# Kernel tuning notes

Measured on AMD Instinct MI355X. Metric: run time of the kernel, lower is better.

## Reference

```python
import jax, jax.numpy as jnp
import numpy as np

B, T, C, H = 4, 2048, 768, 12
HD = C // H
EPS = 1e-5

def _ln(x, s, b):
    m = jnp.mean(x, axis=-1, keepdims=True)
    v = jnp.mean(jnp.square(x - m), axis=-1, keepdims=True)
    return (x - m) * jax.lax.rsqrt(v + EPS) * s + b

def setup_inputs() -> dict:
    key = jax.random.key(0)
    ks = jax.random.split(key, 8)
    x = jax.random.normal(ks[0], (B, T, C), dtype=jnp.float32)
    mask = jnp.tril(jnp.ones((T, T), dtype=bool))[None, None, :, :]  # causal [1,1,T,T]
    s = lambda fan_in: 1.0 / np.sqrt(fan_in)
    return {
        "x": x,
        "mask": mask,
        "ln1_s": jnp.ones((C,), jnp.float32),
        "ln1_b": jnp.zeros((C,), jnp.float32),
        "w_attn": jax.random.normal(ks[1], (C, 3 * C), jnp.float32) * s(C),
        "b_attn": jnp.zeros((3 * C,), jnp.float32),
        "w_o": jax.random.normal(ks[2], (C, C), jnp.float32) * s(C),
        "b_o": jnp.zeros((C,), jnp.float32),
        "ln2_s": jnp.ones((C,), jnp.float32),
        "ln2_b": jnp.zeros((C,), jnp.float32),
        "w_fc": jax.random.normal(ks[3], (C, 4 * C), jnp.float32) * s(C),
        "b_fc": jnp.zeros((4 * C,), jnp.float32),
        "w_proj": jax.random.normal(ks[4], (4 * C, C), jnp.float32) * s(4 * C),
        "b_proj": jnp.zeros((C,), jnp.float32),
    }

def reference(x, mask, ln1_s, ln1_b, w_attn, b_attn, w_o, b_o,
              ln2_s, ln2_b, w_fc, b_fc, w_proj, b_proj):
    # --- attention branch (pre-LN) ---
    h = _ln(x, ln1_s, ln1_b)
    qkv = (h @ w_attn + b_attn).reshape(B, T, 3 * H, HD)
    q, k, v = jnp.array_split(qkv, 3, axis=2)  # each [B,T,H,HD]
    scale = 1.0 / jnp.sqrt(jnp.float32(HD))
    attn = jnp.einsum('bqhd,bkhd->bhqk', q, k) * scale
    attn = jnp.where(mask, attn, jnp.finfo(jnp.float32).min)
    attn = jax.nn.softmax(attn, axis=-1)
    ctx = jnp.einsum('bhqk,bkhd->bqhd', attn, v).reshape(B, T, C)
    x = x + ctx @ w_o + b_o
    # --- MLP branch (pre-LN) ---
    h = _ln(x, ln2_s, ln2_b)
    h = jax.nn.gelu(h @ w_fc + b_fc, approximate=True)
    x = x + h @ w_proj + b_proj
    return x
```

## Files before the change

### kernel.cpp

```cpp
#include <hip/hip_runtime.h>


typedef unsigned short u16;
typedef unsigned int u32;
typedef __attribute__((ext_vector_type(8))) short short8;
typedef __attribute__((ext_vector_type(4))) float f32x4;
typedef __attribute__((ext_vector_type(16))) float f32x16;

__device__ __forceinline__ u16 f2bf(float f) {
    union { float f; unsigned u; } v; v.f = f;
    unsigned u = v.u;
    unsigned r = (u + 0x7FFFu + ((u >> 16) & 1u)) >> 16;
    return (u16)r;
}
__device__ __forceinline__ float bf2f(u16 h) {
    union { u32 u; float f; } v; v.u = ((u32)h) << 16;
    return v.f;
}

__device__ __forceinline__ u32 cvtpk_bf16(float lo, float hi) {
    u32 r;
    asm("v_cvt_pk_bf16_f32 %0, %1, %2" : "=v"(r) : "v"(lo), "v"(hi));
    return r;
}

__device__ __forceinline__ void gld16(const u16* g, u16* l) {
    __builtin_amdgcn_global_load_lds(
        (const __attribute__((address_space(1))) void*)g,
        (__attribute__((address_space(3))) void*)l, 16, 0, 0);
}

__device__ __forceinline__ float gelu_fast(float v) {
    float t = v * v;
    float z2n = v * (-2.3022078f - 0.10294376f * t);
    float e = __builtin_amdgcn_exp2f(z2n);
    return v * __builtin_amdgcn_rcpf(1.0f + e);
}

__device__ __forceinline__ void ln_core(float v0, float v1, float v2,
                                        const float* __restrict__ s,
                                        const float* __restrict__ b,
                                        u16* __restrict__ orow,
                                        float* red, int tid) {
    float sum = v0 + v1 + v2;
    float sq = v0 * v0 + v1 * v1 + v2 * v2;
#pragma unroll
    for (int off = 32; off; off >>= 1) {
        sum += __shfl_down(sum, off);
        sq += __shfl_down(sq, off);
    }
    int wid = tid >> 6, lane = tid & 63;
    if (lane == 0) { red[wid] = sum; red[4 + wid] = sq; }
    __syncthreads();
    if (tid == 0) {
        float s4 = red[0] + red[1] + red[2] + red[3];
        float q4 = red[4] + red[5] + red[6] + red[7];
        red[0] = s4 * (1.0f / 768.0f);
        red[1] = q4 * (1.0f / 768.0f);
    }
    __syncthreads();
    float mean = red[0];
    float var = red[1] - mean * mean;
    float rstd = rsqrtf(var + 1e-5f);
    orow[tid]       = f2bf((v0 - mean) * rstd * s[tid]       + b[tid]);
    orow[tid + 256] = f2bf((v1 - mean) * rstd * s[tid + 256] + b[tid + 256]);
    orow[tid + 512] = f2bf((v2 - mean) * rstd * s[tid + 512] + b[tid + 512]);
}

__global__ void pre_kernel(const float* __restrict__ w_attn, u16* __restrict__ wT_attn,
                           const float* __restrict__ w_o,    u16* __restrict__ wT_o,
                           const float* __restrict__ w_fc,   u16* __restrict__ wT_fc,
                           const float* __restrict__ w_proj, u16* __restrict__ wT_proj,
                           const float* __restrict__ x, const float* __restrict__ ln1_s,
                           const float* __restrict__ ln1_b, u16* __restrict__ h) {
    __shared__ float t[32][33];
    __shared__ float red[8];
    int tile = blockIdx.x;
    int tid = threadIdx.x;
    if (tile >= 6912) {
        int row = tile - 6912;
        const float* xr = x + (size_t)row * 768;
        ln_core(xr[tid], xr[tid + 256], xr[tid + 512], ln1_s, ln1_b,
                h + (size_t)row * 768, red, tid);
        return;
    }
    const float* w; u16* wt; int N; int idx;
    if (tile < 1728)      { w = w_attn; wt = wT_attn; N = 2304; idx = tile; }
    else if (tile < 2304) { w = w_o;    wt = wT_o;    N = 768;  idx = tile - 1728; }
    else if (tile < 4608) { w = w_fc;   wt = wT_fc;   N = 3072; idx = tile - 2304; }
    else                  { w = w_proj; wt = wT_proj; N = 768;  idx = tile - 4608; }
    int K = (tile >= 4608) ? 3072 : 768;
    int nx = N / 32;
    int n0 = (idx % nx) * 32, k0 = (idx / nx) * 32;
    int tx = tid & 31, ty = tid >> 5;
#pragma unroll
    for (int i = 0; i < 4; i++)
        t[ty + 8 * i][tx] = w[(size_t)(k0 + ty + 8 * i) * N + n0 + tx];
    __syncthreads();
#pragma unroll
    for (int i = 0; i < 4; i++)
        wt[(size_t)(n0 + ty + 8 * i) * K + k0 + tx] = f2bf(t[tx][ty + 8 * i]);
}

__global__ void ln_bf16_kernel(const u16* __restrict__ x, const float* __restrict__ s,
                               const float* __restrict__ b, u16* __restrict__ out) {
    __shared__ float red[8];
    int row = blockIdx.x;
    int tid = threadIdx.x;
    const u16* xr = x + (size_t)row * 768;
    ln_core(bf2f(xr[tid]), bf2f(xr[tid + 256]), bf2f(xr[tid + 512]),
            s, b, out + (size_t)row * 768, red, tid);
}

template <int GELU, int RES, int RESBF, int OUTMODE, int BM>
__global__ __launch_bounds__(256) void gemm_kernel(
    const u16* __restrict__ A, const u16* __restrict__ Wt,
    const float* __restrict__ bias, const void* __restrict__ res,
    void* __restrict__ out, int M, int N, int K,
    u16* __restrict__ qbuf, u16* __restrict__ kbuf, u16* __restrict__ vbuf) {
    constexpr int FM = BM / 32;
    constexpr int SA = BM / 32;
    constexpr int WR = BM / 2;
    __shared__ __align__(16) u16 lA[2][BM * 64];
    __shared__ __align__(16) u16 lB[2][128 * 64];
    int m0 = blockIdx.x * BM, n0 = blockIdx.y * 128;
    int tid = threadIdx.x;
    int wid = tid >> 6, lane = tid & 63;
    int wr = wid >> 1, wc = wid & 1;
    int l15 = lane & 15, lhi = lane >> 4;

    const u16* aptr[SA];
    const u16* bptr[4];
#pragma unroll
    for (int s = 0; s < SA; s++) {
        int u = s * 256 + tid;
        int row = u >> 3;
        int c8 = (u & 7) ^ (row & 7);
        aptr[s] = A + (size_t)(m0 + row) * K + c8 * 8;
    }
#pragma unroll
    for (int s = 0; s < 4; s++) {
        int u = s * 256 + tid;
        int row = u >> 3;
        int c8 = (u & 7) ^ (row & 7);
        bptr[s] = Wt + (size_t)(n0 + row) * K + c8 * 8;
    }

    f32x4 acc[FM][4];
#pragma unroll
    for (int i = 0; i < FM; i++)
#pragma unroll
        for (int j = 0; j < 4; j++) acc[i][j] = (f32x4)0.0f;

#pragma unroll
    for (int s = 0; s < SA; s++) gld16(aptr[s], &lA[0][(s * 256 + tid) * 8]);
#pragma unroll
    for (int s = 0; s < 4; s++) gld16(bptr[s], &lB[0][(s * 256 + tid) * 8]);
    __syncthreads();

    int KT = K >> 6;
    int cur = 0;
    for (int t = 0; t < KT; t++) {
        if (t + 1 < KT) {
            int ko = (t + 1) << 6;
#pragma unroll
            for (int s = 0; s < SA; s++) gld16(aptr[s] + ko, &lA[cur ^ 1][(s * 256 + tid) * 8]);
#pragma unroll
            for (int s = 0; s < 4; s++) gld16(bptr[s] + ko, &lB[cur ^ 1][(s * 256 + tid) * 8]);
        }
        short8 af[2][FM], bfr[2][4];
#pragma unroll
        for (int ks = 0; ks < 2; ks++) {
#pragma unroll
            for (int f = 0; f < FM; f++) {
                int ra = wr * WR + f * 16 + l15;
                af[ks][f] = *(const short8*)&lA[cur][ra * 64 + (((ks * 4 + lhi) ^ (ra & 7)) << 3)];
            }
#pragma unroll
            for (int f = 0; f < 4; f++) {
                int rb = wc * 64 + f * 16 + l15;
                bfr[ks][f] = *(const short8*)&lB[cur][rb * 64 + (((ks * 4 + lhi) ^ (rb & 7)) << 3)];
            }
        }
        __builtin_amdgcn_s_setprio(1);
#pragma unroll
        for (int ks = 0; ks < 2; ks++)
#pragma unroll
            for (int fm = 0; fm < FM; fm++)
#pragma unroll
                for (int fn = 0; fn < 4; fn++)
                    acc[fm][fn] = __builtin_amdgcn_mfma_f32_16x16x32_bf16(
                        af[ks][fm], bfr[ks][fn], acc[fm][fn], 0, 0, 0);
        __builtin_amdgcn_s_setprio(0);
        __syncthreads();
        cur ^= 1;
    }

    if (OUTMODE == 2) {
        int region = n0 / 768;
#pragma unroll
        for (int fm = 0; fm < FM; fm++)
#pragma unroll
            for (int fn = 0; fn < 4; fn++) {
                int col = n0 + wc * 64 + fn * 16 + l15;
                float bv = bias[col];
                int c = col - region * 768;
                int h = c >> 6, d = c & 63;
                if (region == 2) {
                    int row0 = m0 + wr * WR + fm * 16 + lhi * 4;
                    int bb = row0 >> 11, t0 = row0 & 2047;
                    size_t bh = (size_t)bb * 12 + h;
                    union { u16 a[4]; uint2 v; } pk;
#pragma unroll
                    for (int r = 0; r < 4; r++) pk.a[r] = f2bf(acc[fm][fn][r] + bv);
                    *(uint2*)(&vbuf[(bh * 64 + d) * 2048 + t0]) = pk.v;
                } else {
#pragma unroll
                    for (int r = 0; r < 4; r++) {
                        int row = m0 + wr * WR + fm * 16 + lhi * 4 + r;
                        int bb = row >> 11, t = row & 2047;
                        u16 val = f2bf(acc[fm][fn][r] + bv);
                        size_t bh = (size_t)bb * 12 + h;
                        if (region == 0) qbuf[(bh * 2048 + t) * 64 + d] = val;
                        else             kbuf[(bh * 2048 + t) * 64 + d] = val;
                    }
                }
            }
    } else {
#pragma unroll
        for (int fm = 0; fm < FM; fm++)
#pragma unroll
            for (int fn = 0; fn < 4; fn++) {
                int col = n0 + wc * 64 + fn * 16 + l15;
                float bv = bias[col];
#pragma unroll
                for (int r = 0; r < 4; r++) {
                    int row = m0 + wr * WR + fm * 16 + lhi * 4 + r;
                    float v = acc[fm][fn][r] + bv;
                    if (RES) {
                        if (RESBF) v += bf2f(((const u16*)res)[(size_t)row * N + col]);
                        else       v += ((const float*)res)[(size_t)row * N + col];
                    }
                    if (GELU) v = gelu_fast(v);
                    if (OUTMODE == 1)
                        ((u16*)out)[(size_t)row * N + col] = f2bf(v);
                    else
                        ((float*)out)[(size_t)row * N + col] = v;
                }
            }
    }
}

__global__ __launch_bounds__(128) void attn_kernel(const u16* __restrict__ qbuf,
                                                   const u16* __restrict__ kbuf,
                                                   const u16* __restrict__ vbuf,
                                                   u16* __restrict__ ctx) {
    int bid = blockIdx.x;
    int qt = 31 - (bid / 48);
    int bh = bid % 48;
    int b = bh / 12, h = bh % 12;
    int q0 = qt * 64;
    int tid = threadIdx.x, wid = tid >> 6, lane = tid & 63;
    int l31 = lane & 31, hi = lane >> 5;

    __shared__ __align__(16) u16 lK[2][64 * 64];
    __shared__ __align__(16) u16 lV[2][64 * 64];

    const size_t bhT = (size_t)bh * 2048;

    const u16* kp[4];
    const u16* vp[4];
#pragma unroll
    for (int s = 0; s < 4; s++) {
        int u = s * 128 + tid;
        int row = u >> 3;
        int c8 = (u & 7) ^ (row & 7);
        kp[s] = kbuf + (bhT + row) * 64 + c8 * 8;
        vp[s] = vbuf + ((size_t)bh * 64 + row) * 2048 + c8 * 8;
    }

    int qrow = q0 + wid * 32 + l31;
    short8 bq[4];
#pragma unroll
    for (int ks = 0; ks < 4; ks++)
        bq[ks] = *(const short8*)(qbuf + (bhT + qrow) * 64 + ks * 16 + hi * 8);

    short8 ones;
#pragma unroll
    for (int j = 0; j < 8; j++) ones[j] = (short)0x3F80;

    f32x16 oacc[2], sacc;
#pragma unroll
    for (int dt = 0; dt < 2; dt++) oacc[dt] = (f32x16)0.0f;
    sacc = (f32x16)0.0f;
    float mb = -1e30f;
    const float C2 = 0.125f * 1.44269504089f;
    const float THR = 11.55f;
    int myq = q0 + wid * 32 + l31;

    int nt = qt + 1;
#pragma unroll
    for (int s = 0; s < 4; s++) gld16(kp[s], &lK[0][(s * 128 + tid) * 8]);
#pragma unroll
    for (int s = 0; s < 4; s++) gld16(vp[s], &lV[0][(s * 128 + tid) * 8]);
    __syncthreads();

    int cur = 0;
    for (int t = 0; t < nt; t++) {
        int k0 = t * 64;
        if (t + 1 < nt) {
            int kn = (t + 1) * 64;
#pragma unroll
            for (int s = 0; s < 4; s++) gld16(kp[s] + (size_t)kn * 64, &lK[cur ^ 1][(s * 128 + tid) * 8]);
#pragma unroll
            for (int s = 0; s < 4; s++) gld16(vp[s] + kn, &lV[cur ^ 1][(s * 128 + tid) * 8]);
        }
        {
            f32x16 sa[2];
#pragma unroll
            for (int kt = 0; kt < 2; kt++) sa[kt] = (f32x16)0.0f;
            __builtin_amdgcn_s_setprio(1);
#pragma unroll
            for (int kt = 0; kt < 2; kt++) {
                int rk = kt * 32 + l31;
#pragma unroll
                for (int ks = 0; ks < 4; ks++) {
                    short8 ak = *(const short8*)&lK[cur][rk * 64 + (((ks * 2 + hi) ^ (rk & 7)) << 3)];
                    sa[kt] = __builtin_amdgcn_mfma_f32_32x32x16_bf16(ak, bq[ks], sa[kt], 0, 0, 0);
                }
            }
            __builtin_amdgcn_s_setprio(0);
            if (k0 + 63 > q0 + wid * 32) {
#pragma unroll
                for (int kt = 0; kt < 2; kt++)
#pragma unroll
                    for (int r = 0; r < 16; r++) {
                        int key = k0 + kt * 32 + (r & 3) + 8 * (r >> 2) + 4 * hi;
                        if (key > myq) sa[kt][r] = -1e30f;
                    }
            }
            float tmax = -1e30f;
#pragma unroll
            for (int kt = 0; kt < 2; kt++)
#pragma unroll
                for (int r = 0; r < 16; r += 2)
                    tmax = fmaxf(tmax, fmaxf(sa[kt][r], sa[kt][r + 1]));
            tmax = fmaxf(tmax, __shfl_xor(tmax, 32));
            float tmb = tmax * C2;
            if (__any(tmb > mb + THR)) {
                float mbn = fmaxf(mb, tmb);
                float corr = __builtin_amdgcn_exp2f(mb - mbn);
#pragma unroll
                for (int r = 0; r < 16; r++) {
                    int qm = (r & 3) + 8 * (r >> 2) + 4 * hi;
                    float c = __shfl(corr, qm);
                    oacc[0][r] *= c;
                    oacc[1][r] *= c;
                    sacc[r] *= c;
                }
                mb = mbn;
            }
#pragma unroll
            for (int kt = 0; kt < 2; kt++)
#pragma unroll
                for (int r = 0; r < 16; r++)
                    sa[kt][r] = __builtin_amdgcn_exp2f(fmaf(sa[kt][r], C2, -mb));
            short8 pa[4];
#pragma unroll
            for (int kt = 0; kt < 2; kt++)
#pragma unroll
                for (int ks2 = 0; ks2 < 2; ks2++) {
                    int base = ks2 * 8;
                    u32 A0 = cvtpk_bf16(sa[kt][base + 0], sa[kt][base + 1]);
                    u32 B0 = cvtpk_bf16(sa[kt][base + 4], sa[kt][base + 5]);
                    u32 A1 = cvtpk_bf16(sa[kt][base + 2], sa[kt][base + 3]);
                    u32 B1 = cvtpk_bf16(sa[kt][base + 6], sa[kt][base + 7]);
                    u32 A0s = (u32)__shfl_xor((int)A0, 32);
                    u32 B0s = (u32)__shfl_xor((int)B0, 32);
                    u32 A1s = (u32)__shfl_xor((int)A1, 32);
                    u32 B1s = (u32)__shfl_xor((int)B1, 32);
                    union { u32 u[4]; short8 s; } w;
                    w.u[0] = hi ? B0s : A0;
                    w.u[1] = hi ? B1s : A1;
                    w.u[2] = hi ? B0 : A0s;
                    w.u[3] = hi ? B1 : A1s;
                    pa[kt * 2 + ks2] = w.s;
                }
            __builtin_amdgcn_s_setprio(1);
#pragma unroll
            for (int kt = 0; kt < 2; kt++)
#pragma unroll
                for (int ks2 = 0; ks2 < 2; ks2++) {
                    short8 ap = pa[kt * 2 + ks2];
#pragma unroll
                    for (int dt = 0; dt < 2; dt++) {
                        int rd = dt * 32 + l31;
                        short8 bv = *(const short8*)&lV[cur][rd * 64 + (((kt * 4 + ks2 * 2 + hi) ^ (rd & 7)) << 3)];
                        oacc[dt] = __builtin_amdgcn_mfma_f32_32x32x16_bf16(ap, bv, oacc[dt], 0, 0, 0);
                    }
                    sacc = __builtin_amdgcn_mfma_f32_32x32x16_bf16(ap, ones, sacc, 0, 0, 0);
                }
            __builtin_amdgcn_s_setprio(0);
        }
        __syncthreads();
        cur ^= 1;
    }
    const size_t rowb = (size_t)b * 2048;
#pragma unroll
    for (int r = 0; r < 16; r++) {
        float ir = __builtin_amdgcn_rcpf(sacc[r]);
        int qm = (r & 3) + 8 * (r >> 2) + 4 * hi;
        int row = q0 + wid * 32 + qm;
        u16* op = ctx + (rowb + row) * 768 + h * 64 + l31;
        op[0]  = f2bf(oacc[0][r] * ir);
        op[32] = f2bf(oacc[1][r] * ir);
    }
}

extern "C" void kernel_launch(void* const* d_in, const int* in_sizes, int n_in,
                              void* d_out, int out_size, void* d_ws, size_t ws_size,
                              hipStream_t stream) {
    const float* x      = (const float*)d_in[0];
    const float* ln1_s  = (const float*)d_in[2];
    const float* ln1_b  = (const float*)d_in[3];
    const float* w_attn = (const float*)d_in[4];
    const float* b_attn = (const float*)d_in[5];
    const float* w_o    = (const float*)d_in[6];
    const float* b_o    = (const float*)d_in[7];
    const float* ln2_s  = (const float*)d_in[8];
    const float* ln2_b  = (const float*)d_in[9];
    const float* w_fc   = (const float*)d_in[10];
    const float* b_fc   = (const float*)d_in[11];
    const float* w_proj = (const float*)d_in[12];
    const float* b_proj = (const float*)d_in[13];

    char* ws = (char*)d_ws;
    u16* wT_attn = (u16*)(ws + 0);
    u16* wT_o    = (u16*)(ws + 3538944);
    u16* wT_fc   = (u16*)(ws + 4718592);
    u16* wT_proj = (u16*)(ws + 9437184);
    u16* bufA    = (u16*)(ws + 14155776);
    u16* qbuf    = (u16*)(ws + 26738688);
    u16* kbuf    = (u16*)(ws + 39321600);
    u16* vbuf    = (u16*)(ws + 51904512);
    u16* act     = (u16*)(ws + 26738688);
    u16* x1b     = (u16*)(ws + 77070336);

    pre_kernel<<<15104, 256, 0, stream>>>(w_attn, wT_attn, w_o, wT_o, w_fc, wT_fc,
                                          w_proj, wT_proj, x, ln1_s, ln1_b, bufA);
    gemm_kernel<0, 0, 0, 2, 128><<<dim3(64, 18), 256, 0, stream>>>(bufA, wT_attn, b_attn, nullptr, nullptr,
                                                                   8192, 2304, 768, qbuf, kbuf, vbuf);
    attn_kernel<<<1536, 128, 0, stream>>>(qbuf, kbuf, vbuf, bufA);
    gemm_kernel<0, 1, 0, 1, 64><<<dim3(128, 6), 256, 0, stream>>>(bufA, wT_o, b_o, x, x1b,
                                                                  8192, 768, 768, nullptr, nullptr, nullptr);
    ln_bf16_kernel<<<8192, 256, 0, stream>>>(x1b, ln2_s, ln2_b, bufA);
    gemm_kernel<1, 0, 0, 1, 128><<<dim3(64, 24), 256, 0, stream>>>(bufA, wT_fc, b_fc, nullptr, act,
                                                                   8192, 3072, 768, nullptr, nullptr, nullptr);
    gemm_kernel<0, 1, 1, 0, 64><<<dim3(128, 6), 256, 0, stream>>>(act, wT_proj, b_proj, x1b, (float*)d_out,
                                                                  8192, 768, 3072, nullptr, nullptr, nullptr);
}
```

Baseline: 252.6 us.

## Load attention K tiles directly into registers instead of shared memory

The attention kernel no longer stages K through double-buffered LDS. Each lane loads its MFMA A-operand fragments for the next K tile straight from global memory into a register double-buffer (ak0/ak1), alternating by tile parity. V is still staged through LDS. This removes the LDS write/read traffic for K and frees LDS, but it raises register pressure (16 short8 held live) and duplicates global K loads across the two waves, which may lower occupancy or expose load latency.

```diff
diff --git a/kernel.cpp b/kernel.cpp
--- a/kernel.cpp
+++ b/kernel.cpp
@@ -263,21 +263,19 @@
     int tid = threadIdx.x, wid = tid >> 6, lane = tid & 63;
     int l31 = lane & 31, hi = lane >> 5;
 
-    __shared__ __align__(16) u16 lK[2][64 * 64];
     __shared__ __align__(16) u16 lV[2][64 * 64];
 
     const size_t bhT = (size_t)bh * 2048;
 
-    const u16* kp[4];
     const u16* vp[4];
 #pragma unroll
     for (int s = 0; s < 4; s++) {
         int u = s * 128 + tid;
         int row = u >> 3;
         int c8 = (u & 7) ^ (row & 7);
-        kp[s] = kbuf + (bhT + row) * 64 + c8 * 8;
         vp[s] = vbuf + ((size_t)bh * 64 + row) * 2048 + c8 * 8;
     }
+    const u16* kb = kbuf + bhT * 64 + (size_t)l31 * 64 + hi * 8;
 
     int qrow = q0 + wid * 32 + l31;
     short8 bq[4];
@@ -299,112 +297,120 @@
     int myq = q0 + wid * 32 + l31;
 
     int nt = qt + 1;
-#pragma unroll
-    for (int s = 0; s < 4; s++) gld16(kp[s], &lK[0][(s * 128 + tid) * 8]);
-#pragma unroll
-    for (int s = 0; s < 4; s++) gld16(vp[s], &lV[0][(s * 128 + tid) * 8]);
-    __syncthreads();
+    short8 ak0[8], ak1[8];
+
+    auto loadK = [&](short8* ak, int k0) {
+#pragma unroll
+        for (int kt = 0; kt < 2; kt++)
+#pragma unroll
+            for (int ks = 0; ks < 4; ks++)
+                ak[kt * 4 + ks] = *(const short8*)(kb + (size_t)(k0 + kt * 32) * 64 + ks * 16);
+    };
 
     int cur = 0;
-    for (int t = 0; t < nt; t++) {
+    auto tile_body = [&](short8* akC, short8* akN, int t) {
         int k0 = t * 64;
         if (t + 1 < nt) {
             int kn = (t + 1) * 64;
-#pragma unroll
-            for (int s = 0; s < 4; s++) gld16(kp[s] + (size_t)kn * 64, &lK[cur ^ 1][(s * 128 + tid) * 8]);
+            loadK(akN, kn);
 #pragma unroll
             for (int s = 0; s < 4; s++) gld16(vp[s] + kn, &lV[cur ^ 1][(s * 128 + tid) * 8]);
         }
-        {
-            f32x16 sa[2];
-#pragma unroll
-            for (int kt = 0; kt < 2; kt++) sa[kt] = (f32x16)0.0f;
-            __builtin_amdgcn_s_setprio(1);
-#pragma unroll
-            for (int kt = 0; kt < 2; kt++) {
-                int rk = kt * 32 + l31;
-#pragma unroll
-                for (int ks = 0; ks < 4; ks++) {
-                    short8 ak = *(const short8*)&lK[cur][rk * 64 + (((ks * 2 + hi) ^ (rk & 7)) << 3)];
-                    sa[kt] = __builtin_amdgcn_mfma_f32_32x32x16_bf16(ak, bq[ks], sa[kt], 0, 0, 0);
+        f32x16 sa[2];
+#pragma unroll
+        for (int kt = 0; kt < 2; kt++) sa[kt] = (f32x16)0.0f;
+        __builtin_amdgcn_s_setprio(1);
+#pragma unroll
+        for (int kt = 0; kt < 2; kt++)
+#pragma unroll
+            for (int ks = 0; ks < 4; ks++)
+                sa[kt] = __builtin_amdgcn_mfma_f32_32x32x16_bf16(akC[kt * 4 + ks], bq[ks], sa[kt], 0, 0, 0);
+        __builtin_amdgcn_s_setprio(0);
+        if (k0 + 63 > q0 + wid * 32) {
+#pragma unroll
+            for (int kt = 0; kt < 2; kt++)
+#pragma unroll
+                for (int r = 0; r < 16; r++) {
+                    int key = k0 + kt * 32 + (r & 3) + 8 * (r >> 2) + 4 * hi;
+                    if (key > myq) sa[kt][r] = -1e30f;
                 }
-            }
-            __builtin_amdgcn_s_setprio(0);
-            if (k0 + 63 > q0 + wid * 32) {
-#pragma unroll
-                for (int kt = 0; kt < 2; kt++)
-#pragma unroll
-                    for (int r = 0; r < 16; r++) {
-                        int key = k0 + kt * 32 + (r & 3) + 8 * (r >> 2) + 4 * hi;
-                        if (key > myq) sa[kt][r] = -1e30f;
-                    }
-            }
-            float tmax = -1e30f;
-#pragma unroll
-            for (int kt = 0; kt < 2; kt++)
-#pragma unroll
-                for (int r = 0; r < 16; r += 2)
-                    tmax = fmaxf(tmax, fmaxf(sa[kt][r], sa[kt][r + 1]));
-            tmax = fmaxf(tmax, __shfl_xor(tmax, 32));
-            float tmb = tmax * C2;
-            if (__any(tmb > mb + THR)) {
-                float mbn = fmaxf(mb, tmb);
-                float corr = __builtin_amdgcn_exp2f(mb - mbn);
-#pragma unroll
-                for (int r = 0; r < 16; r++) {
-                    int qm = (r & 3) + 8 * (r >> 2) + 4 * hi;
-                    float c = __shfl(corr, qm);
-                    oacc[0][r] *= c;
-                    oacc[1][r] *= c;
-                    sacc[r] *= c;
+        }
+        float tmax = -1e30f;
+#pragma unroll
+        for (int kt = 0; kt < 2; kt++)
+#pragma unroll
+            for (int r = 0; r < 16; r += 2)
+                tmax = fmaxf(tmax, fmaxf(sa[kt][r], sa[kt][r + 1]));
+        tmax = fmaxf(tmax, __shfl_xor(tmax, 32));
+        float tmb = tmax * C2;
+        if (__any(tmb > mb + THR)) {
+            float mbn = fmaxf(mb, tmb);
+            float corr = __builtin_amdgcn_exp2f(mb - mbn);
+#pragma unroll
+            for (int r = 0; r < 16; r++) {
+                int qm = (r & 3) + 8 * (r >> 2) + 4 * hi;
+                float c = __shfl(corr, qm);
+                oacc[0][r] *= c;
+                oacc[1][r] *= c;
+                sacc[r] *= c;
+            }
+            mb = mbn;
+        }
+#pragma unroll
+        for (int kt = 0; kt < 2; kt++)
+#pragma unroll
+            for (int r = 0; r < 16; r++)
+                sa[kt][r] = __builtin_amdgcn_exp2f(fmaf(sa[kt][r], C2, -mb));
+        short8 pa[4];
+#pragma unroll
+        for (int kt = 0; kt < 2; kt++)
+#pragma unroll
+            for (int ks2 = 0; ks2 < 2; ks2++) {
+                int base = ks2 * 8;
+                u32 A0 = cvtpk_bf16(sa[kt][base + 0], sa[kt][base + 1]);
+                u32 B0 = cvtpk_bf16(sa[kt][base + 4], sa[kt][base + 5]);
+                u32 A1 = cvtpk_bf16(sa[kt][base + 2], sa[kt][base + 3]);
+                u32 B1 = cvtpk_bf16(sa[kt][base + 6], sa[kt][base + 7]);
+                u32 A0s = (u32)__shfl_xor((int)A0, 32);
+                u32 B0s = (u32)__shfl_xor((int)B0, 32);
+                u32 A1s = (u32)__shfl_xor((int)A1, 32);
+                u32 B1s = (u32)__shfl_xor((int)B1, 32);
+                union { u32 u[4]; short8 s; } w;
+                w.u[0] = hi ? B0s : A0;
+                w.u[1] = hi ? B1s : A1;
+                w.u[2] = hi ? B0 : A0s;
+                w.u[3] = hi ? B1 : A1s;
+                pa[kt * 2 + ks2] = w.s;
+            }
+        __builtin_amdgcn_s_setprio(1);
+#pragma unroll
+        for (int kt = 0; kt < 2; kt++)
+#pragma unroll
+            for (int ks2 = 0; ks2 < 2; ks2++) {
+                short8 ap = pa[kt * 2 + ks2];
+#pragma unroll
+                for (int dt = 0; dt < 2; dt++) {
+                    int rd = dt * 32 + l31;
+                    short8 bv = *(const short8*)&lV[cur][rd * 64 + (((kt * 4 + ks2 * 2 + hi) ^ (rd & 7)) << 3)];
+                    oacc[dt] = __builtin_amdgcn_mfma_f32_32x32x16_bf16(ap, bv, oacc[dt], 0, 0, 0);
                 }
-                mb = mbn;
-            }
-#pragma unroll
-            for (int kt = 0; kt < 2; kt++)
-#pragma unroll
-                for (int r = 0; r < 16; r++)
-                    sa[kt][r] = __builtin_amdgcn_exp2f(fmaf(sa[kt][r], C2, -mb));
-            short8 pa[4];
-#pragma unroll
-            for (int kt = 0; kt < 2; kt++)
-#pragma unroll
-                for (int ks2 = 0; ks2 < 2; ks2++) {
-                    int base = ks2 * 8;
-                    u32 A0 = cvtpk_bf16(sa[kt][base + 0], sa[kt][base + 1]);
-                    u32 B0 = cvtpk_bf16(sa[kt][base + 4], sa[kt][base + 5]);
-                    u32 A1 = cvtpk_bf16(sa[kt][base + 2], sa[kt][base + 3]);
-                    u32 B1 = cvtpk_bf16(sa[kt][base + 6], sa[kt][base + 7]);
-                    u32 A0s = (u32)__shfl_xor((int)A0, 32);
-                    u32 B0s = (u32)__shfl_xor((int)B0, 32);
-                    u32 A1s = (u32)__shfl_xor((int)A1, 32);
-                    u32 B1s = (u32)__shfl_xor((int)B1, 32);
-                    union { u32 u[4]; short8 s; } w;
-                    w.u[0] = hi ? B0s : A0;
-                    w.u[1] = hi ? B1s : A1;
-                    w.u[2] = hi ? B0 : A0s;
-                    w.u[3] = hi ? B1 : A1s;
-                    pa[kt * 2 + ks2] = w.s;
-                }
-            __builtin_amdgcn_s_setprio(1);
-#pragma unroll
-            for (int kt = 0; kt < 2; kt++)
-#pragma unroll
-                for (int ks2 = 0; ks2 < 2; ks2++) {
-                    short8 ap = pa[kt * 2 + ks2];
-#pragma unroll
-                    for (int dt = 0; dt < 2; dt++) {
-                        int rd = dt * 32 + l31;
-                        short8 bv = *(const short8*)&lV[cur][rd * 64 + (((kt * 4 + ks2 * 2 + hi) ^ (rd & 7)) << 3)];
-                        oacc[dt] = __builtin_amdgcn_mfma_f32_32x32x16_bf16(ap, bv, oacc[dt], 0, 0, 0);
-                    }
-                    sacc = __builtin_amdgcn_mfma_f32_32x32x16_bf16(ap, ones, sacc, 0, 0, 0);
-                }
-            __builtin_amdgcn_s_setprio(0);
-        }
+                sacc = __builtin_amdgcn_mfma_f32_32x32x16_bf16(ap, ones, sacc, 0, 0, 0);
+            }
+        __builtin_amdgcn_s_setprio(0);
+    };
+
+    loadK(ak0, 0);
+#pragma unroll
+    for (int s = 0; s < 4; s++) gld16(vp[s], &lV[0][(s * 128 + tid) * 8]);
+    __syncthreads();
+
+    for (int t = 0; t < nt; t++) {
+        if (t & 1) tile_body(ak1, ak0, t);
+        else       tile_body(ak0, ak1, t);
         __syncthreads();
         cur ^= 1;
     }
+
     const size_t rowb = (size_t)b * 2048;
 #pragma unroll
     for (int r = 0; r < 16; r++) {
```

Measured after the change: 324.9 us. 28.7% more time.

## Add 256x256-tile GEMM kernel for MLP FC layer with GELU

Applied to the files above, without the earlier changes.

Adds a dedicated 512-thread GEMM kernel with 256x256 output tiles, double-buffered LDS staging with swizzled layout, and a fused bias+GELU bf16 epilogue, and uses it for the MLP up-projection. Larger tiles raise arithmetic intensity and cut global/LDS load traffic per MFMA. In exchange the grid shrinks to 384 blocks with 128KB LDS each, so occupancy is one block per CU and wave quantization may leave CUs idle in the tail.

```diff
diff --git a/kernel.cpp b/kernel.cpp
--- a/kernel.cpp
+++ b/kernel.cpp
@@ -249,6 +249,100 @@
                 }
             }
     }
+}
+
+template <int GELU>
+__global__ __launch_bounds__(512) void gemm256_kernel(
+    const u16* __restrict__ A, const u16* __restrict__ Wt,
+    const float* __restrict__ bias, u16* __restrict__ out,
+    int M, int N, int K) {
+    __shared__ __align__(16) u16 lA[2][256 * 64];
+    __shared__ __align__(16) u16 lB[2][256 * 64];
+    int m0 = blockIdx.x * 256, n0 = blockIdx.y * 256;
+    int tid = threadIdx.x;
+    int wid = tid >> 6, lane = tid & 63;
+    int wr = wid >> 2, wc = wid & 3;
+    int l15 = lane & 15, lhi = lane >> 4;
+
+    const u16* aptr[4];
+    const u16* bptr[4];
+#pragma unroll
+    for (int s = 0; s < 4; s++) {
+        int u = s * 512 + tid;
+        int row = u >> 3;
+        int c8 = (u & 7) ^ (row & 7);
+        aptr[s] = A + (size_t)(m0 + row) * K + c8 * 8;
+        bptr[s] = Wt + (size_t)(n0 + row) * K + c8 * 8;
+    }
+
+    auto stage = [&](int t, int buf) {
+        int ko = t << 6;
+#pragma unroll
+        for (int s = 0; s < 4; s++) gld16(aptr[s] + ko, &lA[buf][(s * 512 + tid) * 8]);
+#pragma unroll
+        for (int s = 0; s < 4; s++) gld16(bptr[s] + ko, &lB[buf][(s * 512 + tid) * 8]);
+    };
+
+    f32x4 acc[8][4];
+#pragma unroll
+    for (int i = 0; i < 8; i++)
+#pragma unroll
+        for (int j = 0; j < 4; j++) acc[i][j] = (f32x4)0.0f;
+
+    int KT = K >> 6;
+    stage(0, 0);
+    stage(1, 1);
+
+    int cur = 0;
+    for (int t = 0; t < KT; t++) {
+        if (t + 1 < KT) asm volatile("s_waitcnt vmcnt(8)" ::: "memory");
+        else            asm volatile("s_waitcnt vmcnt(0)" ::: "memory");
+        __builtin_amdgcn_s_barrier();
+        __builtin_amdgcn_sched_barrier(0);
+
+#pragma unroll
+        for (int ks = 0; ks < 2; ks++) {
+            short8 af[8], bfr[4];
+#pragma unroll
+            for (int f = 0; f < 8; f++) {
+                int ra = wr * 128 + f * 16 + l15;
+                af[f] = *(const short8*)&lA[cur][ra * 64 + (((ks * 4 + lhi) ^ (ra & 7)) << 3)];
+            }
+#pragma unroll
+            for (int f = 0; f < 4; f++) {
+                int rb = wc * 64 + f * 16 + l15;
+                bfr[f] = *(const short8*)&lB[cur][rb * 64 + (((ks * 4 + lhi) ^ (rb & 7)) << 3)];
+            }
+            __builtin_amdgcn_s_setprio(1);
+#pragma unroll
+            for (int fm = 0; fm < 8; fm++)
+#pragma unroll
+                for (int fn = 0; fn < 4; fn++)
+                    acc[fm][fn] = __builtin_amdgcn_mfma_f32_16x16x32_bf16(
+                        af[fm], bfr[fn], acc[fm][fn], 0, 0, 0);
+            __builtin_amdgcn_s_setprio(0);
+        }
+        __builtin_amdgcn_sched_barrier(0);
+        __builtin_amdgcn_s_barrier();
+        __builtin_amdgcn_sched_barrier(0);
+        if (t + 2 < KT) stage(t + 2, cur);
+        cur ^= 1;
+    }
+
+#pragma unroll
+    for (int fm = 0; fm < 8; fm++)
+#pragma unroll
+        for (int fn = 0; fn < 4; fn++) {
+            int col = n0 + wc * 64 + fn * 16 + l15;
+            float bv = bias[col];
+#pragma unroll
+            for (int r = 0; r < 4; r++) {
+                int row = m0 + wr * 128 + fm * 16 + lhi * 4 + r;
+                float v = acc[fm][fn][r] + bv;
+                if (GELU) v = gelu_fast(v);
+                out[(size_t)row * N + col] = f2bf(v);
+            }
+        }
 }
 
 __global__ __launch_bounds__(128) void attn_kernel(const u16* __restrict__ qbuf,
@@ -454,8 +548,7 @@
     gemm_kernel<0, 1, 0, 1, 64><<<dim3(128, 6), 256, 0, stream>>>(bufA, wT_o, b_o, x, x1b,
                                                                   8192, 768, 768, nullptr, nullptr, nullptr);
     ln_bf16_kernel<<<8192, 256, 0, stream>>>(x1b, ln2_s, ln2_b, bufA);
-    gemm_kernel<1, 0, 0, 1, 128><<<dim3(64, 24), 256, 0, stream>>>(bufA, wT_fc, b_fc, nullptr, act,
-                                                                   8192, 3072, 768, nullptr, nullptr, nullptr);
+    gemm256_kernel<1><<<dim3(32, 12), 512, 0, stream>>>(bufA, wT_fc, b_fc, act, 8192, 3072, 768);
     gemm_kernel<0, 1, 1, 0, 64><<<dim3(128, 6), 256, 0, stream>>>(act, wT_proj, b_proj, x1b, (float*)d_out,
                                                                   8192, 768, 3072, nullptr, nullptr, nullptr);
 }
```

Result: slower. 258.6 us (+2.4%).
